# Kernel optimization log

Measured on AMD Instinct MI355X. Metric: run time of the kernel, lower is better.

The kernel has to match this reference:

```python
import jax, jax.numpy as jnp
import numpy as np

B, S, D, H, DK, DV = 2, 2048, 1024, 16, 64, 64
EPS = 1e-6

def setup_inputs() -> dict:
    key = jax.random.key(0)
    ks = jax.random.split(key, 5)
    sc = 1.0 / np.sqrt(D)
    return {
        "ip": jax.random.normal(ks[0], (B, S, D), jnp.float32),
        "wk": jax.random.normal(ks[1], (D, H * DK), jnp.float32) * sc,
        "wq": jax.random.normal(ks[2], (D, H * DK), jnp.float32) * sc,
        "wv": jax.random.normal(ks[3], (D, H * DV), jnp.float32) * sc,
        "fc_w": jax.random.normal(ks[4], (H * DV, D), jnp.float32) * (1.0 / np.sqrt(H * DV)),
        "fc_b": jnp.zeros((D,), jnp.float32),
        "ln_g": jnp.ones((D,), jnp.float32),
        "ln_b": jnp.zeros((D,), jnp.float32),
    }

def reference(ip, wk, wq, wv, fc_w, fc_b, ln_g, ln_b):
    m, t, _ = ip.shape
    temp = jnp.asarray(DK ** 0.5, ip.dtype)
    # projections -> [m, t, H, d]
    k = (ip @ wk).reshape(m, t, H, DK)
    q = (ip @ wq).reshape(m, t, H, DK)
    v = (ip @ wv).reshape(m, t, H, DV)
    # scores [m, H, t, t]; dropout is identity in eval mode
    scores = jnp.einsum('mqhd,mkhd->mhqk', q, k) / temp
    attn = jax.nn.softmax(scores, axis=-1)
    # context [m, t, H*DV]
    ctx = jnp.einsum('mhqk,mkhd->mqhd', attn, v).reshape(m, t, H * DV)
    out = ctx @ fc_w + fc_b + ip  # fc + residual
    # LayerNorm over last dim (biased variance, eps=1e-6)
    mu = jnp.mean(out, axis=-1, keepdims=True)
    var = jnp.mean(jnp.square(out - mu), axis=-1, keepdims=True)
    y = (out - mu) * jax.lax.rsqrt(var + EPS) * ln_g + ln_b
    return (y, attn)
```

## Files before the change

kernel.cpp:

```cpp
#include <hip/hip_runtime.h>
#include <hip/hip_bf16.h>
#include <stdint.h>

#define S_LEN 2048
#define DMODEL 1024
#define NH 16
#define HD 64
#define SC2 0.18033688011112042f

typedef __attribute__((ext_vector_type(8))) short bf16x8;
typedef __attribute__((ext_vector_type(4))) float f32x4;
typedef unsigned long long u64;

__device__ __forceinline__ void gload16(const void* g, void* l) {
  __builtin_amdgcn_global_load_lds(
      reinterpret_cast<const __attribute__((address_space(1))) void*>(reinterpret_cast<uintptr_t>(g)),
      reinterpret_cast<__attribute__((address_space(3))) void*>(reinterpret_cast<uintptr_t>(l)),
      16, 0, 0);
}

__device__ __forceinline__ f32x4 mfma_bf16(bf16x8 a, bf16x8 b, f32x4 c) {
  return __builtin_amdgcn_mfma_f32_16x16x32_bf16(a, b, c, 0, 0, 0);
}

__device__ __forceinline__ unsigned short bfbits(float x) {
  __hip_bfloat16 h = __float2bfloat16(x);
  return *reinterpret_cast<unsigned short*>(&h);
}

__device__ __forceinline__ float asf(unsigned u) {
  union { unsigned u; float f; } c; c.u = u; return c.f;
}

__device__ __forceinline__ void wait_vm0_bar() {
  __builtin_amdgcn_sched_barrier(0);
  asm volatile("s_waitcnt vmcnt(0) lgkmcnt(0)" ::: "memory");
  __builtin_amdgcn_s_barrier();
  __builtin_amdgcn_sched_barrier(0);
}
__device__ __forceinline__ void wait_vm2_bar() {
  __builtin_amdgcn_sched_barrier(0);
  asm volatile("s_waitcnt vmcnt(2) lgkmcnt(0)" ::: "memory");
  __builtin_amdgcn_s_barrier();
  __builtin_amdgcn_sched_barrier(0);
}
__device__ __forceinline__ void wait_vm4_bar() {
  __builtin_amdgcn_sched_barrier(0);
  asm volatile("s_waitcnt vmcnt(4) lgkmcnt(0)" ::: "memory");
  __builtin_amdgcn_s_barrier();
  __builtin_amdgcn_sched_barrier(0);
}

__global__ __launch_bounds__(256) void k_prep(const float* __restrict__ ip,
                                              const float* __restrict__ wq,
                                              const float* __restrict__ wk,
                                              const float* __restrict__ wv,
                                              const float* __restrict__ fcw,
                                              __hip_bfloat16* __restrict__ ipb,
                                              __hip_bfloat16* __restrict__ wt_all,
                                              __hip_bfloat16* __restrict__ fct) {
  int bid = blockIdx.x;
  if (bid < 4096) {
    int i = (bid * 256 + threadIdx.x) * 4;
    f32x4 v = *(const f32x4*)(ip + i);
    u64 p = (u64)bfbits(v[0]) | ((u64)bfbits(v[1]) << 16) | ((u64)bfbits(v[2]) << 32)
          | ((u64)bfbits(v[3]) << 48);
    *reinterpret_cast<u64*>(ipb + i) = p;
    return;
  }
  bid -= 4096;
  const int z = bid >> 10, tile_id = bid & 1023;
  const float* src = (z == 0) ? wq : (z == 1) ? wk : (z == 2) ? wv : fcw;
  __hip_bfloat16* dst = (z == 3) ? fct : wt_all + (size_t)z * DMODEL * DMODEL;
  __shared__ float tile[32][33];
  const int nb = (tile_id & 31) * 32, kb = (tile_id >> 5) * 32;
  const int lx = threadIdx.x & 31, ly = threadIdx.x >> 5;
#pragma unroll
  for (int i = 0; i < 4; ++i)
    tile[ly + 8 * i][lx] = src[(size_t)(kb + ly + 8 * i) * DMODEL + nb + lx];
  __syncthreads();
#pragma unroll
  for (int i = 0; i < 4; ++i)
    dst[(size_t)(nb + ly + 8 * i) * DMODEL + kb + lx] = __float2bfloat16(tile[lx][ly + 8 * i]);
}

template <int MODE>
__global__ __launch_bounds__(256) void k_gemm(const __hip_bfloat16* __restrict__ A,
                                              const __hip_bfloat16* __restrict__ Bt,
                                              __hip_bfloat16* __restrict__ Q,
                                              __hip_bfloat16* __restrict__ Kk,
                                              __hip_bfloat16* __restrict__ Vt,
                                              const __hip_bfloat16* __restrict__ resid,
                                              const float* __restrict__ bias,
                                              float* __restrict__ preln) {
  __shared__ __align__(128) char lds[16384];
  char* Al = lds;
  char* Bl = lds + 8192;
  const int t = threadIdx.x;
  const int w = t >> 6, l = t & 63;
  const int g = l >> 4, lr = l & 15;
  const int cpx = gridDim.x >> 3;
  const int swz = (blockIdx.x & 7) * cpx + (blockIdx.x >> 3);
  const int bm = swz & 31;
  const int bn = swz >> 5;

  int sr0 = (w * 2 + 0) * 16 + (l >> 2);
  int sr1 = (w * 2 + 1) * 16 + (l >> 2);
  const int sc = (l & 3) * 16;
  const char* aSrc0 = (const char*)A + ((size_t)(bm * 128 + sr0)) * 2048 + (sc ^ (((sr0 >> 1) & 3) << 4));
  const char* aSrc1 = (const char*)A + ((size_t)(bm * 128 + sr1)) * 2048 + (sc ^ (((sr1 >> 1) & 3) << 4));
  const char* bSrc0 = (const char*)Bt + ((size_t)(bn * 128 + sr0)) * 2048 + (sc ^ (((sr0 >> 1) & 3) << 4));
  const char* bSrc1 = (const char*)Bt + ((size_t)(bn * 128 + sr1)) * 2048 + (sc ^ (((sr1 >> 1) & 3) << 4));

  const int wm = (w >> 1) * 64, wn = (w & 1) * 64;
  int roff[4], noff[4];
#pragma unroll
  for (int mi = 0; mi < 4; ++mi) {
    int m = wm + mi * 16 + lr;
    roff[mi] = m * 64 + ((g * 16) ^ (((m >> 1) & 3) << 4));
  }
#pragma unroll
  for (int ni = 0; ni < 4; ++ni) {
    int n = wn + ni * 16 + lr;
    noff[ni] = n * 64 + ((g * 16) ^ (((n >> 1) & 3) << 4));
  }

  f32x4 acc[4][4] = {};
  for (int k0 = 0; k0 < DMODEL; k0 += 32) {
    gload16(aSrc0 + k0 * 2, Al + (w * 2 + 0) * 1024);
    gload16(aSrc1 + k0 * 2, Al + (w * 2 + 1) * 1024);
    gload16(bSrc0 + k0 * 2, Bl + (w * 2 + 0) * 1024);
    gload16(bSrc1 + k0 * 2, Bl + (w * 2 + 1) * 1024);
    __syncthreads();
    bf16x8 af[4], bfv[4];
#pragma unroll
    for (int mi = 0; mi < 4; ++mi) af[mi] = *(const bf16x8*)(Al + roff[mi]);
#pragma unroll
    for (int ni = 0; ni < 4; ++ni) bfv[ni] = *(const bf16x8*)(Bl + noff[ni]);
#pragma unroll
    for (int mi = 0; mi < 4; ++mi)
#pragma unroll
      for (int ni = 0; ni < 4; ++ni)
        acc[mi][ni] = mfma_bf16(af[mi], bfv[ni], acc[mi][ni]);
    __syncthreads();
  }

#pragma unroll
  for (int mi = 0; mi < 4; ++mi)
#pragma unroll
    for (int ni = 0; ni < 4; ++ni) {
      f32x4 v = acc[mi][ni];
      const int m0 = bm * 128 + wm + mi * 16 + g * 4;
      const int n = bn * 128 + wn + ni * 16 + lr;
      if (MODE == 0) {
        const int mat = n >> 10, c = n & 1023;
        const int h = c >> 6, d = c & 63;
        const int b = m0 >> 11, s0 = m0 & 2047;
        if (mat == 2) {
          u64 p = (u64)bfbits(v[0]) | ((u64)bfbits(v[1]) << 16) | ((u64)bfbits(v[2]) << 32)
                | ((u64)bfbits(v[3]) << 48);
          *reinterpret_cast<u64*>(Vt + ((size_t)(b * NH + h) * HD + d) * S_LEN + s0) = p;
        } else {
          __hip_bfloat16* dst = (mat == 0) ? Q : Kk;
#pragma unroll
          for (int r = 0; r < 4; ++r)
            dst[(((size_t)(b * NH + h)) * S_LEN + s0 + r) * HD + d] = __float2bfloat16(v[r]);
        }
      } else {
#pragma unroll
        for (int r = 0; r < 4; ++r) {
          size_t idx = (size_t)(m0 + r) * DMODEL + n;
          preln[idx] = v[r] + bias[n] + __bfloat162float(resid[idx]);
        }
      }
    }
}

__global__ __launch_bounds__(256, 2) void k_attn8(const __hip_bfloat16* __restrict__ Q,
                                                  const __hip_bfloat16* __restrict__ K,
                                                  const __hip_bfloat16* __restrict__ Vt,
                                                  float* __restrict__ attn,
                                                  __hip_bfloat16* __restrict__ ctx) {
  __shared__ __align__(128) char KVst[4][8192];
  __shared__ __align__(128) char Pw[2][4][4096];

  const int t = threadIdx.x, w = t >> 6, l = t & 63;
  const int g = l >> 4, lr = l & 15;
  const int bid = blockIdx.x;
  const int bh = bid & 31, qi = bid >> 5;
  const int b = bh >> 4, h = bh & 15;
  const int q0 = qi * 64 + w * 16;
  const char* Kh = (const char*)(K + (size_t)bh * S_LEN * HD);
  const char* Vh = (const char*)(Vt + (size_t)bh * HD * S_LEN);
  const __hip_bfloat16* Qh = Q + (size_t)bh * S_LEN * HD;

  bf16x8 qf0 = *(const bf16x8*)(Qh + (size_t)(q0 + lr) * HD + 8 * g);
  bf16x8 qf1 = *(const bf16x8*)(Qh + (size_t)(q0 + lr) * HD + 32 + 8 * g);

  const int srow0 = w * 8 + (l >> 3), srow1 = srow0 + 32;
  const int sb = (l & 7) * 16;
  const int kso0 = srow0 * 128 + (sb ^ ((srow0 & 7) << 4));
  const int kso1 = srow1 * 128 + (sb ^ ((srow1 & 7) << 4));
  const int vso0 = srow0 * 4096 + (sb ^ ((srow0 & 7) << 4));
  const int vso1 = srow1 * 4096 + (sb ^ ((srow1 & 7) << 4));
  const int swz = (lr & 7) << 4;

  gload16(Kh + kso0, &KVst[0][w * 1024]);
  gload16(Kh + kso1, &KVst[0][4096 + w * 1024]);
  gload16(Kh + 8192 + kso0, &KVst[1][w * 1024]);
  gload16(Kh + 8192 + kso1, &KVst[1][4096 + w * 1024]);
  float lsum = 0.f;
#define P1_COMPUTE(c)                                                              \
  {                                                                                \
    const char* kb_ = &KVst[(c) & 3][0];                                           \
    _Pragma("unroll") for (int st = 0; st < 4; ++st) {                             \
      const char* kr = kb_ + (st * 16 + lr) * 128;                                 \
      bf16x8 kf0 = *(const bf16x8*)(kr + ((g * 16) ^ swz));                        \
      bf16x8 kf1 = *(const bf16x8*)(kr + ((64 + g * 16) ^ swz));                   \
      f32x4 s = {};                                                                \
      s = mfma_bf16(kf0, qf0, s);                                                  \
      s = mfma_bf16(kf1, qf1, s);                                                  \
      lsum += __builtin_amdgcn_exp2f(s[0] * SC2) + __builtin_amdgcn_exp2f(s[1] * SC2) \
            + __builtin_amdgcn_exp2f(s[2] * SC2) + __builtin_amdgcn_exp2f(s[3] * SC2); \
    }                                                                              \
  }
  for (int c = 0; c < 30; ++c) {
    gload16(Kh + (c + 2) * 8192 + kso0, &KVst[(c + 2) & 3][w * 1024]);
    gload16(Kh + (c + 2) * 8192 + kso1, &KVst[(c + 2) & 3][4096 + w * 1024]);
    wait_vm4_bar();
    P1_COMPUTE(c);
  }
  wait_vm2_bar();
  P1_COMPUTE(30);
  wait_vm0_bar();
  P1_COMPUTE(31);
#undef P1_COMPUTE
  lsum += __shfl_xor(lsum, 16);
  lsum += __shfl_xor(lsum, 32);
  const float inv = 1.0f / lsum;

  gload16(Kh + kso0, &KVst[0][w * 1024]);
  gload16(Kh + kso1, &KVst[0][4096 + w * 1024]);
  gload16(Vh + vso0, &KVst[2][w * 1024]);
  gload16(Vh + vso1, &KVst[2][4096 + w * 1024]);
  wait_vm0_bar();

  f32x4 o[4] = {};
  const size_t arowbase = ((size_t)bh * S_LEN + q0) * S_LEN;
  const int sl_row = l >> 5, sl_col = l & 31;
  for (int c = 0; c < 32; ++c) {
    const int cur = c & 1;
    const int gbuf = (c >> 1) & 1;
    const int ce = c & 1;
    if (c < 31) {
      gload16(Kh + (c + 1) * 8192 + kso0, &KVst[cur ^ 1][w * 1024]);
      gload16(Kh + (c + 1) * 8192 + kso1, &KVst[cur ^ 1][4096 + w * 1024]);
      gload16(Vh + (c + 1) * 128 + vso0, &KVst[2 + (cur ^ 1)][w * 1024]);
      gload16(Vh + (c + 1) * 128 + vso1, &KVst[2 + (cur ^ 1)][4096 + w * 1024]);
    }
    if (c >= 2) {
      const char* psrc = &Pw[gbuf ^ 1][w][0];
      const int kvb = ((c >> 1) - 1) * 128;
#pragma unroll
      for (int i = 0; i < 4; ++i) {
        int row = ce * 8 + 2 * i + sl_row;
        u64 v = *reinterpret_cast<const u64*>(psrc + row * 256 + ((sl_col * 8) ^ ((row & 7) << 4)));
        unsigned lo = (unsigned)v, hi = (unsigned)(v >> 32);
        f32x4 pv;
        pv[0] = asf(lo << 16);
        pv[1] = asf(lo & 0xffff0000u);
        pv[2] = asf(hi << 16);
        pv[3] = asf(hi & 0xffff0000u);
        __builtin_nontemporal_store(pv, (f32x4*)(attn + arowbase + (size_t)row * S_LEN + kvb + sl_col * 4));
      }
    }
#pragma unroll
    for (int st = 0; st < 4; ++st) {
      const char* kr = &KVst[cur][(st * 16 + lr) * 128];
      bf16x8 kf0 = *(const bf16x8*)(kr + ((g * 16) ^ swz));
      bf16x8 kf1 = *(const bf16x8*)(kr + ((64 + g * 16) ^ swz));
      f32x4 s = {};
      s = mfma_bf16(kf0, qf0, s);
      s = mfma_bf16(kf1, qf1, s);
      float p0 = __builtin_amdgcn_exp2f(s[0] * SC2) * inv;
      float p1 = __builtin_amdgcn_exp2f(s[1] * SC2) * inv;
      float p2 = __builtin_amdgcn_exp2f(s[2] * SC2) * inv;
      float p3 = __builtin_amdgcn_exp2f(s[3] * SC2) * inv;
      u64 u = (u64)bfbits(p0) | ((u64)bfbits(p1) << 16) | ((u64)bfbits(p2) << 32)
            | ((u64)bfbits(p3) << 48);
      *reinterpret_cast<u64*>(&Pw[gbuf][w][lr * 256 + ((ce * 128 + st * 32 + g * 8) ^ swz)]) = u;
    }
    __builtin_amdgcn_s_setprio(1);
#pragma unroll
    for (int ks = 0; ks < 2; ++ks) {
      bf16x8 pf = *(const bf16x8*)(&Pw[gbuf][w][lr * 256 + ((ce * 128 + ks * 64 + g * 16) ^ swz)]);
#pragma unroll
      for (int dvt = 0; dvt < 4; ++dvt) {
        const char* vb = &KVst[2 + cur][(dvt * 16 + lr) * 128];
        bf16x8 vf = *(const bf16x8*)(vb + ((ks * 64 + g * 16) ^ swz));
        o[dvt] = mfma_bf16(pf, vf, o[dvt]);
      }
    }
    __builtin_amdgcn_s_setprio(0);
    if (c < 31) wait_vm4_bar();
  }

  {
    const char* psrc = &Pw[1][w][0];
#pragma unroll
    for (int i = 0; i < 8; ++i) {
      int row = 2 * i + sl_row;
      u64 v = *reinterpret_cast<const u64*>(psrc + row * 256 + ((sl_col * 8) ^ ((row & 7) << 4)));
      unsigned lo = (unsigned)v, hi = (unsigned)(v >> 32);
      f32x4 pv;
      pv[0] = asf(lo << 16);
      pv[1] = asf(lo & 0xffff0000u);
      pv[2] = asf(hi << 16);
      pv[3] = asf(hi & 0xffff0000u);
      __builtin_nontemporal_store(pv, (f32x4*)(attn + arowbase + (size_t)row * S_LEN + 1920 + sl_col * 4));
    }
  }

#pragma unroll
  for (int dvt = 0; dvt < 4; ++dvt)
#pragma unroll
    for (int r = 0; r < 4; ++r) {
      int q = q0 + g * 4 + r;
      size_t idx = ((size_t)b * S_LEN + q) * DMODEL + h * HD + dvt * 16 + lr;
      ctx[idx] = __float2bfloat16(o[dvt][r]);
    }
}

__global__ __launch_bounds__(256) void k_ln(const float* __restrict__ x,
                                            const float* __restrict__ gam,
                                            const float* __restrict__ bet,
                                            float* __restrict__ y) {
  const int row = blockIdx.x;
  const int i = threadIdx.x * 4;
  const float* xr = x + (size_t)row * DMODEL;
  f32x4 v = *(const f32x4*)(xr + i);
  float s = v[0] + v[1] + v[2] + v[3];
  float s2 = v[0] * v[0] + v[1] * v[1] + v[2] * v[2] + v[3] * v[3];
#pragma unroll
  for (int off = 1; off < 64; off <<= 1) {
    s += __shfl_xor(s, off);
    s2 += __shfl_xor(s2, off);
  }
  __shared__ float red[2][4];
  const int w = threadIdx.x >> 6, ln = threadIdx.x & 63;
  if (ln == 0) { red[0][w] = s; red[1][w] = s2; }
  __syncthreads();
  s = red[0][0] + red[0][1] + red[0][2] + red[0][3];
  s2 = red[1][0] + red[1][1] + red[1][2] + red[1][3];
  const float mu = s * (1.f / DMODEL);
  const float rstd = rsqrtf(s2 * (1.f / DMODEL) - mu * mu + 1e-6f);
  f32x4 gv = *(const f32x4*)(gam + i), bv = *(const f32x4*)(bet + i);
  f32x4 out;
#pragma unroll
  for (int j = 0; j < 4; ++j) out[j] = (v[j] - mu) * rstd * gv[j] + bv[j];
  *(f32x4*)(y + (size_t)row * DMODEL + i) = out;
}

extern "C" void kernel_launch(void* const* d_in, const int* in_sizes, int n_in,
                              void* d_out, int out_size, void* d_ws, size_t ws_size,
                              hipStream_t stream) {
  const float* ip  = (const float*)d_in[0];
  const float* wk  = (const float*)d_in[1];
  const float* wq  = (const float*)d_in[2];
  const float* wv  = (const float*)d_in[3];
  const float* fcw = (const float*)d_in[4];
  const float* fcb = (const float*)d_in[5];
  const float* lng = (const float*)d_in[6];
  const float* lnb = (const float*)d_in[7];

  float* y = (float*)d_out;
  float* attn = y + (size_t)2 * S_LEN * DMODEL;

  char* ws = (char*)d_ws;
  __hip_bfloat16* ipb = (__hip_bfloat16*)(ws);
  __hip_bfloat16* wt  = (__hip_bfloat16*)(ws + (8ll << 20));
  __hip_bfloat16* fct = (__hip_bfloat16*)(ws + (14ll << 20));
  __hip_bfloat16* Qb  = (__hip_bfloat16*)(ws + (16ll << 20));
  __hip_bfloat16* Kb  = (__hip_bfloat16*)(ws + (24ll << 20));
  __hip_bfloat16* Vtb = (__hip_bfloat16*)(ws + (40ll << 20));
  __hip_bfloat16* ctx = (__hip_bfloat16*)(ws + (48ll << 20));
  float* preln        = (float*)(ws + (56ll << 20));

  k_prep<<<8192, 256, 0, stream>>>(ip, wq, wk, wv, fcw, ipb, wt, fct);
  k_gemm<0><<<32 * 24, 256, 0, stream>>>(ipb, wt, Qb, Kb, Vtb, nullptr, nullptr, nullptr);
  k_attn8<<<1024, 256, 0, stream>>>(Qb, Kb, Vtb, attn, ctx);
  k_gemm<1><<<32 * 8, 256, 0, stream>>>(ctx, fct, nullptr, nullptr, nullptr, ipb, fcb, preln);
  k_ln<<<4096, 256, 0, stream>>>(preln, lng, lnb, y);
}
```

Measured before the change: 211.8 us.

## Warp-specialize attention: split row-sum pass across halves, dedicate warps to attn stores

The attention kernel now launches 512 threads per block instead of 256. In the first pass, the two halves of the block each cover half of the key sequence for the softmax row sums, and the partial sums are combined through shared memory. In the second pass, four warps compute QK, exp and PV, while the other four warps only stream the bf16 probability tiles out to the fp32 attention matrix, so global stores overlap with compute. The pipeline is now single-lookahead double buffering with full vmcnt(0) waits and extra barriers, which may add stalls. The larger blocks also raise register and occupancy pressure.

```diff
diff --git a/kernel.cpp b/kernel.cpp
--- a/kernel.cpp
+++ b/kernel.cpp
@@ -38,15 +38,9 @@
   __builtin_amdgcn_s_barrier();
   __builtin_amdgcn_sched_barrier(0);
 }
-__device__ __forceinline__ void wait_vm2_bar() {
+__device__ __forceinline__ void bar_lgkm() {
   __builtin_amdgcn_sched_barrier(0);
-  asm volatile("s_waitcnt vmcnt(2) lgkmcnt(0)" ::: "memory");
-  __builtin_amdgcn_s_barrier();
-  __builtin_amdgcn_sched_barrier(0);
-}
-__device__ __forceinline__ void wait_vm4_bar() {
-  __builtin_amdgcn_sched_barrier(0);
-  asm volatile("s_waitcnt vmcnt(4) lgkmcnt(0)" ::: "memory");
+  asm volatile("s_waitcnt lgkmcnt(0)" ::: "memory");
   __builtin_amdgcn_s_barrier();
   __builtin_amdgcn_sched_barrier(0);
 }
@@ -176,20 +170,22 @@
     }
 }
 
-__global__ __launch_bounds__(256, 2) void k_attn8(const __hip_bfloat16* __restrict__ Q,
+__global__ __launch_bounds__(512, 4) void k_attn9(const __hip_bfloat16* __restrict__ Q,
                                                   const __hip_bfloat16* __restrict__ K,
                                                   const __hip_bfloat16* __restrict__ Vt,
                                                   float* __restrict__ attn,
                                                   __hip_bfloat16* __restrict__ ctx) {
   __shared__ __align__(128) char KVst[4][8192];
   __shared__ __align__(128) char Pw[2][4][4096];
+  __shared__ float lred[8][16];
 
   const int t = threadIdx.x, w = t >> 6, l = t & 63;
   const int g = l >> 4, lr = l & 15;
   const int bid = blockIdx.x;
   const int bh = bid & 31, qi = bid >> 5;
   const int b = bh >> 4, h = bh & 15;
-  const int q0 = qi * 64 + w * 16;
+  const int wl = w & 3, half = w >> 2;
+  const int q0 = qi * 64 + wl * 16;
   const char* Kh = (const char*)(K + (size_t)bh * S_LEN * HD);
   const char* Vh = (const char*)(Vt + (size_t)bh * HD * S_LEN);
   const __hip_bfloat16* Qh = Q + (size_t)bh * S_LEN * HD;
@@ -197,53 +193,54 @@
   bf16x8 qf0 = *(const bf16x8*)(Qh + (size_t)(q0 + lr) * HD + 8 * g);
   bf16x8 qf1 = *(const bf16x8*)(Qh + (size_t)(q0 + lr) * HD + 32 + 8 * g);
 
-  const int srow0 = w * 8 + (l >> 3), srow1 = srow0 + 32;
-  const int sb = (l & 7) * 16;
-  const int kso0 = srow0 * 128 + (sb ^ ((srow0 & 7) << 4));
-  const int kso1 = srow1 * 128 + (sb ^ ((srow1 & 7) << 4));
-  const int vso0 = srow0 * 4096 + (sb ^ ((srow0 & 7) << 4));
-  const int vso1 = srow1 * 4096 + (sb ^ ((srow1 & 7) << 4));
+  const int srow0 = wl * 8 + (l >> 3), srow1 = srow0 + 32;
+  const int sbt = (l & 7) * 16;
+  const int kso0 = srow0 * 128 + (sbt ^ ((srow0 & 7) << 4));
+  const int kso1 = srow1 * 128 + (sbt ^ ((srow1 & 7) << 4));
+  const int vso0 = srow0 * 4096 + (sbt ^ ((srow0 & 7) << 4));
+  const int vso1 = srow1 * 4096 + (sbt ^ ((srow1 & 7) << 4));
   const int swz = (lr & 7) << 4;
 
-  gload16(Kh + kso0, &KVst[0][w * 1024]);
-  gload16(Kh + kso1, &KVst[0][4096 + w * 1024]);
-  gload16(Kh + 8192 + kso0, &KVst[1][w * 1024]);
-  gload16(Kh + 8192 + kso1, &KVst[1][4096 + w * 1024]);
+  const size_t hbase = (size_t)half * (16 * 8192);
+  gload16(Kh + hbase + kso0, &KVst[half * 2][wl * 1024]);
+  gload16(Kh + hbase + kso1, &KVst[half * 2][4096 + wl * 1024]);
+  wait_vm0_bar();
   float lsum = 0.f;
-#define P1_COMPUTE(c)                                                              \
-  {                                                                                \
-    const char* kb_ = &KVst[(c) & 3][0];                                           \
-    _Pragma("unroll") for (int st = 0; st < 4; ++st) {                             \
-      const char* kr = kb_ + (st * 16 + lr) * 128;                                 \
-      bf16x8 kf0 = *(const bf16x8*)(kr + ((g * 16) ^ swz));                        \
-      bf16x8 kf1 = *(const bf16x8*)(kr + ((64 + g * 16) ^ swz));                   \
-      f32x4 s = {};                                                                \
-      s = mfma_bf16(kf0, qf0, s);                                                  \
-      s = mfma_bf16(kf1, qf1, s);                                                  \
-      lsum += __builtin_amdgcn_exp2f(s[0] * SC2) + __builtin_amdgcn_exp2f(s[1] * SC2) \
-            + __builtin_amdgcn_exp2f(s[2] * SC2) + __builtin_amdgcn_exp2f(s[3] * SC2); \
-    }                                                                              \
-  }
-  for (int c = 0; c < 30; ++c) {
-    gload16(Kh + (c + 2) * 8192 + kso0, &KVst[(c + 2) & 3][w * 1024]);
-    gload16(Kh + (c + 2) * 8192 + kso1, &KVst[(c + 2) & 3][4096 + w * 1024]);
-    wait_vm4_bar();
-    P1_COMPUTE(c);
-  }
-  wait_vm2_bar();
-  P1_COMPUTE(30);
-  wait_vm0_bar();
-  P1_COMPUTE(31);
-#undef P1_COMPUTE
+  for (int c = 0; c < 16; ++c) {
+    if (c < 15) {
+      gload16(Kh + hbase + (c + 1) * 8192 + kso0, &KVst[half * 2 + ((c + 1) & 1)][wl * 1024]);
+      gload16(Kh + hbase + (c + 1) * 8192 + kso1, &KVst[half * 2 + ((c + 1) & 1)][4096 + wl * 1024]);
+    }
+    const char* kb_ = &KVst[half * 2 + (c & 1)][0];
+#pragma unroll
+    for (int st = 0; st < 4; ++st) {
+      const char* kr = kb_ + (st * 16 + lr) * 128;
+      bf16x8 kf0 = *(const bf16x8*)(kr + ((g * 16) ^ swz));
+      bf16x8 kf1 = *(const bf16x8*)(kr + ((64 + g * 16) ^ swz));
+      f32x4 s = {};
+      s = mfma_bf16(kf0, qf0, s);
+      s = mfma_bf16(kf1, qf1, s);
+      lsum += __builtin_amdgcn_exp2f(s[0] * SC2) + __builtin_amdgcn_exp2f(s[1] * SC2)
+            + __builtin_amdgcn_exp2f(s[2] * SC2) + __builtin_amdgcn_exp2f(s[3] * SC2);
+    }
+    wait_vm0_bar();
+  }
   lsum += __shfl_xor(lsum, 16);
   lsum += __shfl_xor(lsum, 32);
-  const float inv = 1.0f / lsum;
-
-  gload16(Kh + kso0, &KVst[0][w * 1024]);
-  gload16(Kh + kso1, &KVst[0][4096 + w * 1024]);
-  gload16(Vh + vso0, &KVst[2][w * 1024]);
-  gload16(Vh + vso1, &KVst[2][4096 + w * 1024]);
-  wait_vm0_bar();
+  if (l < 16) lred[w][l] = lsum;
+  bar_lgkm();
+  float inv = 0.f;
+  if (w < 4) inv = 1.0f / (lred[w][lr] + lred[w + 4][lr]);
+
+  if (w < 4) {
+    gload16(Kh + kso0, &KVst[0][wl * 1024]);
+    gload16(Kh + kso1, &KVst[0][4096 + wl * 1024]);
+    gload16(Vh + vso0, &KVst[2][wl * 1024]);
+    gload16(Vh + vso1, &KVst[2][4096 + wl * 1024]);
+    wait_vm0_bar();
+  } else {
+    bar_lgkm();
+  }
 
   f32x4 o[4] = {};
   const size_t arowbase = ((size_t)bh * S_LEN + q0) * S_LEN;
@@ -252,61 +249,75 @@
     const int cur = c & 1;
     const int gbuf = (c >> 1) & 1;
     const int ce = c & 1;
-    if (c < 31) {
-      gload16(Kh + (c + 1) * 8192 + kso0, &KVst[cur ^ 1][w * 1024]);
-      gload16(Kh + (c + 1) * 8192 + kso1, &KVst[cur ^ 1][4096 + w * 1024]);
-      gload16(Vh + (c + 1) * 128 + vso0, &KVst[2 + (cur ^ 1)][w * 1024]);
-      gload16(Vh + (c + 1) * 128 + vso1, &KVst[2 + (cur ^ 1)][4096 + w * 1024]);
-    }
-    if (c >= 2) {
-      const char* psrc = &Pw[gbuf ^ 1][w][0];
-      const int kvb = ((c >> 1) - 1) * 128;
-#pragma unroll
-      for (int i = 0; i < 4; ++i) {
-        int row = ce * 8 + 2 * i + sl_row;
-        u64 v = *reinterpret_cast<const u64*>(psrc + row * 256 + ((sl_col * 8) ^ ((row & 7) << 4)));
-        unsigned lo = (unsigned)v, hi = (unsigned)(v >> 32);
-        f32x4 pv;
-        pv[0] = asf(lo << 16);
-        pv[1] = asf(lo & 0xffff0000u);
-        pv[2] = asf(hi << 16);
-        pv[3] = asf(hi & 0xffff0000u);
-        __builtin_nontemporal_store(pv, (f32x4*)(attn + arowbase + (size_t)row * S_LEN + kvb + sl_col * 4));
-      }
-    }
-#pragma unroll
-    for (int st = 0; st < 4; ++st) {
-      const char* kr = &KVst[cur][(st * 16 + lr) * 128];
-      bf16x8 kf0 = *(const bf16x8*)(kr + ((g * 16) ^ swz));
-      bf16x8 kf1 = *(const bf16x8*)(kr + ((64 + g * 16) ^ swz));
-      f32x4 s = {};
-      s = mfma_bf16(kf0, qf0, s);
-      s = mfma_bf16(kf1, qf1, s);
-      float p0 = __builtin_amdgcn_exp2f(s[0] * SC2) * inv;
-      float p1 = __builtin_amdgcn_exp2f(s[1] * SC2) * inv;
-      float p2 = __builtin_amdgcn_exp2f(s[2] * SC2) * inv;
-      float p3 = __builtin_amdgcn_exp2f(s[3] * SC2) * inv;
-      u64 u = (u64)bfbits(p0) | ((u64)bfbits(p1) << 16) | ((u64)bfbits(p2) << 32)
-            | ((u64)bfbits(p3) << 48);
-      *reinterpret_cast<u64*>(&Pw[gbuf][w][lr * 256 + ((ce * 128 + st * 32 + g * 8) ^ swz)]) = u;
-    }
-    __builtin_amdgcn_s_setprio(1);
-#pragma unroll
-    for (int ks = 0; ks < 2; ++ks) {
-      bf16x8 pf = *(const bf16x8*)(&Pw[gbuf][w][lr * 256 + ((ce * 128 + ks * 64 + g * 16) ^ swz)]);
-#pragma unroll
-      for (int dvt = 0; dvt < 4; ++dvt) {
-        const char* vb = &KVst[2 + cur][(dvt * 16 + lr) * 128];
-        bf16x8 vf = *(const bf16x8*)(vb + ((ks * 64 + g * 16) ^ swz));
-        o[dvt] = mfma_bf16(pf, vf, o[dvt]);
-      }
-    }
-    __builtin_amdgcn_s_setprio(0);
-    if (c < 31) wait_vm4_bar();
-  }
-
-  {
-    const char* psrc = &Pw[1][w][0];
+    if (w < 4) {
+      if (c < 31) {
+        gload16(Kh + (c + 1) * 8192 + kso0, &KVst[cur ^ 1][wl * 1024]);
+        gload16(Kh + (c + 1) * 8192 + kso1, &KVst[cur ^ 1][4096 + wl * 1024]);
+        gload16(Vh + (c + 1) * 128 + vso0, &KVst[2 + (cur ^ 1)][wl * 1024]);
+        gload16(Vh + (c + 1) * 128 + vso1, &KVst[2 + (cur ^ 1)][4096 + wl * 1024]);
+      }
+#pragma unroll
+      for (int st = 0; st < 4; ++st) {
+        const char* kr = &KVst[cur][(st * 16 + lr) * 128];
+        bf16x8 kf0 = *(const bf16x8*)(kr + ((g * 16) ^ swz));
+        bf16x8 kf1 = *(const bf16x8*)(kr + ((64 + g * 16) ^ swz));
+        f32x4 s = {};
+        s = mfma_bf16(kf0, qf0, s);
+        s = mfma_bf16(kf1, qf1, s);
+        float p0 = __builtin_amdgcn_exp2f(s[0] * SC2) * inv;
+        float p1 = __builtin_amdgcn_exp2f(s[1] * SC2) * inv;
+        float p2 = __builtin_amdgcn_exp2f(s[2] * SC2) * inv;
+        float p3 = __builtin_amdgcn_exp2f(s[3] * SC2) * inv;
+        u64 u = (u64)bfbits(p0) | ((u64)bfbits(p1) << 16) | ((u64)bfbits(p2) << 32)
+              | ((u64)bfbits(p3) << 48);
+        *reinterpret_cast<u64*>(&Pw[gbuf][wl][lr * 256 + ((ce * 128 + st * 32 + g * 8) ^ swz)]) = u;
+      }
+      __builtin_amdgcn_s_setprio(1);
+#pragma unroll
+      for (int ks = 0; ks < 2; ++ks) {
+        bf16x8 pf = *(const bf16x8*)(&Pw[gbuf][wl][lr * 256 + ((ce * 128 + ks * 64 + g * 16) ^ swz)]);
+#pragma unroll
+        for (int dvt = 0; dvt < 4; ++dvt) {
+          const char* vb = &KVst[2 + cur][(dvt * 16 + lr) * 128];
+          bf16x8 vf = *(const bf16x8*)(vb + ((ks * 64 + g * 16) ^ swz));
+          o[dvt] = mfma_bf16(pf, vf, o[dvt]);
+        }
+      }
+      __builtin_amdgcn_s_setprio(0);
+      wait_vm0_bar();
+    } else {
+      if (c >= 2) {
+        const char* psrc = &Pw[gbuf ^ 1][wl][0];
+        const int kvb = ((c >> 1) - 1) * 128;
+#pragma unroll
+        for (int i = 0; i < 4; ++i) {
+          int row = ce * 8 + 2 * i + sl_row;
+          u64 v = *reinterpret_cast<const u64*>(psrc + row * 256 + ((sl_col * 8) ^ ((row & 7) << 4)));
+          unsigned lo = (unsigned)v, hi = (unsigned)(v >> 32);
+          f32x4 pv;
+          pv[0] = asf(lo << 16);
+          pv[1] = asf(lo & 0xffff0000u);
+          pv[2] = asf(hi << 16);
+          pv[3] = asf(hi & 0xffff0000u);
+          __builtin_nontemporal_store(
+              pv, (f32x4*)(attn + arowbase + (size_t)row * S_LEN + kvb + sl_col * 4));
+        }
+      }
+      bar_lgkm();
+    }
+  }
+
+  if (w < 4) {
+#pragma unroll
+    for (int dvt = 0; dvt < 4; ++dvt)
+#pragma unroll
+      for (int r = 0; r < 4; ++r) {
+        int q = q0 + g * 4 + r;
+        size_t idx = ((size_t)b * S_LEN + q) * DMODEL + h * HD + dvt * 16 + lr;
+        ctx[idx] = __float2bfloat16(o[dvt][r]);
+      }
+  } else {
+    const char* psrc = &Pw[1][wl][0];
 #pragma unroll
     for (int i = 0; i < 8; ++i) {
       int row = 2 * i + sl_row;
@@ -320,15 +331,6 @@
       __builtin_nontemporal_store(pv, (f32x4*)(attn + arowbase + (size_t)row * S_LEN + 1920 + sl_col * 4));
     }
   }
-
-#pragma unroll
-  for (int dvt = 0; dvt < 4; ++dvt)
-#pragma unroll
-    for (int r = 0; r < 4; ++r) {
-      int q = q0 + g * 4 + r;
-      size_t idx = ((size_t)b * S_LEN + q) * DMODEL + h * HD + dvt * 16 + lr;
-      ctx[idx] = __float2bfloat16(o[dvt][r]);
-    }
 }
 
 __global__ __launch_bounds__(256) void k_ln(const float* __restrict__ x,
@@ -388,7 +390,7 @@
 
   k_prep<<<8192, 256, 0, stream>>>(ip, wq, wk, wv, fcw, ipb, wt, fct);
   k_gemm<0><<<32 * 24, 256, 0, stream>>>(ipb, wt, Qb, Kb, Vtb, nullptr, nullptr, nullptr);
-  k_attn8<<<1024, 256, 0, stream>>>(Qb, Kb, Vtb, attn, ctx);
+  k_attn9<<<1024, 512, 0, stream>>>(Qb, Kb, Vtb, attn, ctx);
   k_gemm<1><<<32 * 8, 256, 0, stream>>>(ctx, fct, nullptr, nullptr, nullptr, ipb, fcb, preln);
   k_ln<<<4096, 256, 0, stream>>>(preln, lng, lnb, y);
 }
```

New measurement: 213.4 us. No clear change (+0.8%).

## Process two query tiles per attention block, fusing second tile's row-sum pass into first

Applied to the files above, without the earlier changes.

Each attention block now handles 128 queries as two 64-query items instead of 64 queries, halving the grid. The softmax denominator pass for the second item is computed during the first item's main loop, reusing the K tiles already in LDS. This removes one of the two full K sweeps per query tile for half the work. The cost is extra MFMA and exp work in the first item's loop, more register pressure from the extra Q fragments, and fewer blocks to spread across CUs.

```diff
diff --git a/kernel.cpp b/kernel.cpp
--- a/kernel.cpp
+++ b/kernel.cpp
@@ -176,33 +176,35 @@
     }
 }
 
-__global__ __launch_bounds__(256, 2) void k_attn8(const __hip_bfloat16* __restrict__ Q,
-                                                  const __hip_bfloat16* __restrict__ K,
-                                                  const __hip_bfloat16* __restrict__ Vt,
-                                                  float* __restrict__ attn,
-                                                  __hip_bfloat16* __restrict__ ctx) {
+__global__ __launch_bounds__(256, 2) void k_attn10(const __hip_bfloat16* __restrict__ Q,
+                                                   const __hip_bfloat16* __restrict__ K,
+                                                   const __hip_bfloat16* __restrict__ Vt,
+                                                   float* __restrict__ attn,
+                                                   __hip_bfloat16* __restrict__ ctx) {
   __shared__ __align__(128) char KVst[4][8192];
   __shared__ __align__(128) char Pw[2][4][4096];
 
   const int t = threadIdx.x, w = t >> 6, l = t & 63;
   const int g = l >> 4, lr = l & 15;
   const int bid = blockIdx.x;
-  const int bh = bid & 31, qi = bid >> 5;
+  const int bh = bid & 31, qg = bid >> 5;
   const int b = bh >> 4, h = bh & 15;
-  const int q0 = qi * 64 + w * 16;
+  const int qbase = qg * 128;
   const char* Kh = (const char*)(K + (size_t)bh * S_LEN * HD);
   const char* Vh = (const char*)(Vt + (size_t)bh * HD * S_LEN);
   const __hip_bfloat16* Qh = Q + (size_t)bh * S_LEN * HD;
 
-  bf16x8 qf0 = *(const bf16x8*)(Qh + (size_t)(q0 + lr) * HD + 8 * g);
-  bf16x8 qf1 = *(const bf16x8*)(Qh + (size_t)(q0 + lr) * HD + 32 + 8 * g);
+  bf16x8 qa0 = *(const bf16x8*)(Qh + (size_t)(qbase + w * 16 + lr) * HD + 8 * g);
+  bf16x8 qa1 = *(const bf16x8*)(Qh + (size_t)(qbase + w * 16 + lr) * HD + 32 + 8 * g);
+  bf16x8 qb0 = *(const bf16x8*)(Qh + (size_t)(qbase + 64 + w * 16 + lr) * HD + 8 * g);
+  bf16x8 qb1 = *(const bf16x8*)(Qh + (size_t)(qbase + 64 + w * 16 + lr) * HD + 32 + 8 * g);
 
   const int srow0 = w * 8 + (l >> 3), srow1 = srow0 + 32;
-  const int sb = (l & 7) * 16;
-  const int kso0 = srow0 * 128 + (sb ^ ((srow0 & 7) << 4));
-  const int kso1 = srow1 * 128 + (sb ^ ((srow1 & 7) << 4));
-  const int vso0 = srow0 * 4096 + (sb ^ ((srow0 & 7) << 4));
-  const int vso1 = srow1 * 4096 + (sb ^ ((srow1 & 7) << 4));
+  const int sbt = (l & 7) * 16;
+  const int kso0 = srow0 * 128 + (sbt ^ ((srow0 & 7) << 4));
+  const int kso1 = srow1 * 128 + (sbt ^ ((srow1 & 7) << 4));
+  const int vso0 = srow0 * 4096 + (sbt ^ ((srow0 & 7) << 4));
+  const int vso1 = srow1 * 4096 + (sbt ^ ((srow1 & 7) << 4));
   const int swz = (lr & 7) << 4;
 
   gload16(Kh + kso0, &KVst[0][w * 1024]);
@@ -210,19 +212,19 @@
   gload16(Kh + 8192 + kso0, &KVst[1][w * 1024]);
   gload16(Kh + 8192 + kso1, &KVst[1][4096 + w * 1024]);
   float lsum = 0.f;
-#define P1_COMPUTE(c)                                                              \
-  {                                                                                \
-    const char* kb_ = &KVst[(c) & 3][0];                                           \
-    _Pragma("unroll") for (int st = 0; st < 4; ++st) {                             \
-      const char* kr = kb_ + (st * 16 + lr) * 128;                                 \
-      bf16x8 kf0 = *(const bf16x8*)(kr + ((g * 16) ^ swz));                        \
-      bf16x8 kf1 = *(const bf16x8*)(kr + ((64 + g * 16) ^ swz));                   \
-      f32x4 s = {};                                                                \
-      s = mfma_bf16(kf0, qf0, s);                                                  \
-      s = mfma_bf16(kf1, qf1, s);                                                  \
-      lsum += __builtin_amdgcn_exp2f(s[0] * SC2) + __builtin_amdgcn_exp2f(s[1] * SC2) \
+#define P1_COMPUTE(c)                                                                  \
+  {                                                                                    \
+    const char* kb_ = &KVst[(c) & 3][0];                                               \
+    _Pragma("unroll") for (int st = 0; st < 4; ++st) {                                 \
+      const char* kr = kb_ + (st * 16 + lr) * 128;                                     \
+      bf16x8 kf0 = *(const bf16x8*)(kr + ((g * 16) ^ swz));                            \
+      bf16x8 kf1 = *(const bf16x8*)(kr + ((64 + g * 16) ^ swz));                       \
+      f32x4 s = {};                                                                    \
+      s = mfma_bf16(kf0, qa0, s);                                                      \
+      s = mfma_bf16(kf1, qa1, s);                                                      \
+      lsum += __builtin_amdgcn_exp2f(s[0] * SC2) + __builtin_amdgcn_exp2f(s[1] * SC2)  \
             + __builtin_amdgcn_exp2f(s[2] * SC2) + __builtin_amdgcn_exp2f(s[3] * SC2); \
-    }                                                                              \
+    }                                                                                  \
   }
   for (int c = 0; c < 30; ++c) {
     gload16(Kh + (c + 2) * 8192 + kso0, &KVst[(c + 2) & 3][w * 1024]);
@@ -237,7 +239,7 @@
 #undef P1_COMPUTE
   lsum += __shfl_xor(lsum, 16);
   lsum += __shfl_xor(lsum, 32);
-  const float inv = 1.0f / lsum;
+  float inv = 1.0f / lsum;
 
   gload16(Kh + kso0, &KVst[0][w * 1024]);
   gload16(Kh + kso1, &KVst[0][4096 + w * 1024]);
@@ -245,68 +247,104 @@
   gload16(Vh + vso1, &KVst[2][4096 + w * 1024]);
   wait_vm0_bar();
 
+  const int sl_row = l >> 5, sl_col = l & 31;
+  float lsum_nxt = 0.f;
   f32x4 o[4] = {};
-  const size_t arowbase = ((size_t)bh * S_LEN + q0) * S_LEN;
-  const int sl_row = l >> 5, sl_col = l & 31;
-  for (int c = 0; c < 32; ++c) {
-    const int cur = c & 1;
-    const int gbuf = (c >> 1) & 1;
-    const int ce = c & 1;
-    if (c < 31) {
-      gload16(Kh + (c + 1) * 8192 + kso0, &KVst[cur ^ 1][w * 1024]);
-      gload16(Kh + (c + 1) * 8192 + kso1, &KVst[cur ^ 1][4096 + w * 1024]);
-      gload16(Vh + (c + 1) * 128 + vso0, &KVst[2 + (cur ^ 1)][w * 1024]);
-      gload16(Vh + (c + 1) * 128 + vso1, &KVst[2 + (cur ^ 1)][4096 + w * 1024]);
+
+#pragma unroll
+  for (int item = 0; item < 2; ++item) {
+    const bf16x8 qc0 = item ? qb0 : qa0;
+    const bf16x8 qc1 = item ? qb1 : qa1;
+    const int q0 = qbase + item * 64 + w * 16;
+    for (int c = 0; c < 32; ++c) {
+      const int cur = c & 1;
+      const int G = item * 16 + (c >> 1);
+      const int gbuf = (c >> 1) & 1;
+      const int ce = c & 1;
+      const bool lastChunk = (item == 1) && (c == 31);
+      if (!lastChunk) {
+        const int cn = (c + 1) & 31;
+        gload16(Kh + cn * 8192 + kso0, &KVst[cur ^ 1][w * 1024]);
+        gload16(Kh + cn * 8192 + kso1, &KVst[cur ^ 1][4096 + w * 1024]);
+        gload16(Vh + cn * 128 + vso0, &KVst[2 + (cur ^ 1)][w * 1024]);
+        gload16(Vh + cn * 128 + vso1, &KVst[2 + (cur ^ 1)][4096 + w * 1024]);
+      }
+      if (G >= 1) {
+        const int sg = G - 1;
+        const char* psrc = &Pw[sg & 1][w][0];
+        const int kvb = (sg & 15) * 128;
+        const size_t arowbase = ((size_t)bh * S_LEN + qbase + (sg >> 4) * 64 + w * 16) * S_LEN;
+#pragma unroll
+        for (int i = 0; i < 4; ++i) {
+          int row = ce * 8 + 2 * i + sl_row;
+          u64 v = *reinterpret_cast<const u64*>(psrc + row * 256 + ((sl_col * 8) ^ ((row & 7) << 4)));
+          unsigned lo = (unsigned)v, hi = (unsigned)(v >> 32);
+          f32x4 pv;
+          pv[0] = asf(lo << 16);
+          pv[1] = asf(lo & 0xffff0000u);
+          pv[2] = asf(hi << 16);
+          pv[3] = asf(hi & 0xffff0000u);
+          __builtin_nontemporal_store(
+              pv, (f32x4*)(attn + arowbase + (size_t)row * S_LEN + kvb + sl_col * 4));
+        }
+      }
+#pragma unroll
+      for (int st = 0; st < 4; ++st) {
+        const char* kr = &KVst[cur][(st * 16 + lr) * 128];
+        bf16x8 kf0 = *(const bf16x8*)(kr + ((g * 16) ^ swz));
+        bf16x8 kf1 = *(const bf16x8*)(kr + ((64 + g * 16) ^ swz));
+        f32x4 s = {};
+        s = mfma_bf16(kf0, qc0, s);
+        s = mfma_bf16(kf1, qc1, s);
+        float p0 = __builtin_amdgcn_exp2f(s[0] * SC2) * inv;
+        float p1 = __builtin_amdgcn_exp2f(s[1] * SC2) * inv;
+        float p2 = __builtin_amdgcn_exp2f(s[2] * SC2) * inv;
+        float p3 = __builtin_amdgcn_exp2f(s[3] * SC2) * inv;
+        u64 u = (u64)bfbits(p0) | ((u64)bfbits(p1) << 16) | ((u64)bfbits(p2) << 32)
+              | ((u64)bfbits(p3) << 48);
+        *reinterpret_cast<u64*>(&Pw[gbuf][w][lr * 256 + ((ce * 128 + st * 32 + g * 8) ^ swz)]) = u;
+        if (item == 0) {
+          f32x4 sn = {};
+          sn = mfma_bf16(kf0, qb0, sn);
+          sn = mfma_bf16(kf1, qb1, sn);
+          lsum_nxt += __builtin_amdgcn_exp2f(sn[0] * SC2) + __builtin_amdgcn_exp2f(sn[1] * SC2)
+                    + __builtin_amdgcn_exp2f(sn[2] * SC2) + __builtin_amdgcn_exp2f(sn[3] * SC2);
+        }
+      }
+      __builtin_amdgcn_s_setprio(1);
+#pragma unroll
+      for (int ks = 0; ks < 2; ++ks) {
+        bf16x8 pf = *(const bf16x8*)(&Pw[gbuf][w][lr * 256 + ((ce * 128 + ks * 64 + g * 16) ^ swz)]);
+#pragma unroll
+        for (int dvt = 0; dvt < 4; ++dvt) {
+          const char* vb = &KVst[2 + cur][(dvt * 16 + lr) * 128];
+          bf16x8 vf = *(const bf16x8*)(vb + ((ks * 64 + g * 16) ^ swz));
+          o[dvt] = mfma_bf16(pf, vf, o[dvt]);
+        }
+      }
+      __builtin_amdgcn_s_setprio(0);
+      if (!lastChunk) wait_vm4_bar();
     }
-    if (c >= 2) {
-      const char* psrc = &Pw[gbuf ^ 1][w][0];
-      const int kvb = ((c >> 1) - 1) * 128;
-#pragma unroll
-      for (int i = 0; i < 4; ++i) {
-        int row = ce * 8 + 2 * i + sl_row;
-        u64 v = *reinterpret_cast<const u64*>(psrc + row * 256 + ((sl_col * 8) ^ ((row & 7) << 4)));
-        unsigned lo = (unsigned)v, hi = (unsigned)(v >> 32);
-        f32x4 pv;
-        pv[0] = asf(lo << 16);
-        pv[1] = asf(lo & 0xffff0000u);
-        pv[2] = asf(hi << 16);
-        pv[3] = asf(hi & 0xffff0000u);
-        __builtin_nontemporal_store(pv, (f32x4*)(attn + arowbase + (size_t)row * S_LEN + kvb + sl_col * 4));
-      }
+#pragma unroll
+    for (int dvt = 0; dvt < 4; ++dvt)
+#pragma unroll
+      for (int r = 0; r < 4; ++r) {
+        int q = q0 + g * 4 + r;
+        size_t idx = ((size_t)b * S_LEN + q) * DMODEL + h * HD + dvt * 16 + lr;
+        ctx[idx] = __float2bfloat16(o[dvt][r]);
+      }
+    if (item == 0) {
+      lsum_nxt += __shfl_xor(lsum_nxt, 16);
+      lsum_nxt += __shfl_xor(lsum_nxt, 32);
+      inv = 1.0f / lsum_nxt;
+#pragma unroll
+      for (int dvt = 0; dvt < 4; ++dvt) o[dvt] = f32x4{0.f, 0.f, 0.f, 0.f};
     }
-#pragma unroll
-    for (int st = 0; st < 4; ++st) {
-      const char* kr = &KVst[cur][(st * 16 + lr) * 128];
-      bf16x8 kf0 = *(const bf16x8*)(kr + ((g * 16) ^ swz));
-      bf16x8 kf1 = *(const bf16x8*)(kr + ((64 + g * 16) ^ swz));
-      f32x4 s = {};
-      s = mfma_bf16(kf0, qf0, s);
-      s = mfma_bf16(kf1, qf1, s);
-      float p0 = __builtin_amdgcn_exp2f(s[0] * SC2) * inv;
-      float p1 = __builtin_amdgcn_exp2f(s[1] * SC2) * inv;
-      float p2 = __builtin_amdgcn_exp2f(s[2] * SC2) * inv;
-      float p3 = __builtin_amdgcn_exp2f(s[3] * SC2) * inv;
-      u64 u = (u64)bfbits(p0) | ((u64)bfbits(p1) << 16) | ((u64)bfbits(p2) << 32)
-            | ((u64)bfbits(p3) << 48);
-      *reinterpret_cast<u64*>(&Pw[gbuf][w][lr * 256 + ((ce * 128 + st * 32 + g * 8) ^ swz)]) = u;
-    }
-    __builtin_amdgcn_s_setprio(1);
-#pragma unroll
-    for (int ks = 0; ks < 2; ++ks) {
-      bf16x8 pf = *(const bf16x8*)(&Pw[gbuf][w][lr * 256 + ((ce * 128 + ks * 64 + g * 16) ^ swz)]);
-#pragma unroll
-      for (int dvt = 0; dvt < 4; ++dvt) {
-        const char* vb = &KVst[2 + cur][(dvt * 16 + lr) * 128];
-        bf16x8 vf = *(const bf16x8*)(vb + ((ks * 64 + g * 16) ^ swz));
-        o[dvt] = mfma_bf16(pf, vf, o[dvt]);
-      }
-    }
-    __builtin_amdgcn_s_setprio(0);
-    if (c < 31) wait_vm4_bar();
   }
 
   {
     const char* psrc = &Pw[1][w][0];
+    const size_t arowbase = ((size_t)bh * S_LEN + qbase + 64 + w * 16) * S_LEN;
 #pragma unroll
     for (int i = 0; i < 8; ++i) {
       int row = 2 * i + sl_row;
@@ -320,15 +358,6 @@
       __builtin_nontemporal_store(pv, (f32x4*)(attn + arowbase + (size_t)row * S_LEN + 1920 + sl_col * 4));
     }
   }
-
-#pragma unroll
-  for (int dvt = 0; dvt < 4; ++dvt)
-#pragma unroll
-    for (int r = 0; r < 4; ++r) {
-      int q = q0 + g * 4 + r;
-      size_t idx = ((size_t)b * S_LEN + q) * DMODEL + h * HD + dvt * 16 + lr;
-      ctx[idx] = __float2bfloat16(o[dvt][r]);
-    }
 }
 
 __global__ __launch_bounds__(256) void k_ln(const float* __restrict__ x,
@@ -388,7 +417,7 @@
 
   k_prep<<<8192, 256, 0, stream>>>(ip, wq, wk, wv, fcw, ipb, wt, fct);
   k_gemm<0><<<32 * 24, 256, 0, stream>>>(ipb, wt, Qb, Kb, Vtb, nullptr, nullptr, nullptr);
-  k_attn8<<<1024, 256, 0, stream>>>(Qb, Kb, Vtb, attn, ctx);
+  k_attn10<<<512, 256, 0, stream>>>(Qb, Kb, Vtb, attn, ctx);
   k_gemm<1><<<32 * 8, 256, 0, stream>>>(ctx, fct, nullptr, nullptr, nullptr, ipb, fcb, preln);
   k_ln<<<4096, 256, 0, stream>>>(preln, lng, lnb, y);
 }
```

Result: slower. 219.4 us (+3.6%).
